# Kernel optimization log

Measured on AMD Instinct MI355X. Metric: run time of the kernel, lower is better.

## Reference

```python
import jax, jax.numpy as jnp
import numpy as np

D_MODEL = 4096
N_TYPES = 6  # fixed event_types list in the module


def setup_inputs() -> dict:
    key = jax.random.key(0)
    ks = jax.random.split(key, 7)
    E, B, d = 131072, 16384, D_MODEL
    return {
        "event_type": jax.random.randint(ks[0], (E,), 0, N_TYPES),
        "confidence": jax.random.uniform(ks[1], (E,), jnp.float32),
        "location": jax.random.uniform(ks[2], (E, 2), jnp.float32) * jnp.array([640.0, 480.0], jnp.float32),
        "batch_idx": jax.random.randint(ks[3], (E,), 0, B),
        "batch_size": B,
        "type_emb": jax.random.normal(ks[4], (N_TYPES, d // 4), jnp.float32),
        "W1": jax.random.normal(ks[5], (d // 2, d // 4 + 3), jnp.float32) / np.sqrt(d // 4 + 3).astype(np.float32),
        "b1": jnp.zeros((d // 2,), jnp.float32),
        "W2": jax.random.normal(ks[6], (d, d // 2), jnp.float32) / np.sqrt(d // 2).astype(np.float32),
        "b2": jnp.zeros((d,), jnp.float32),
    }


def reference(event_type, confidence, location, batch_idx, batch_size, type_emb, W1, b1, W2, b2):
    E = confidence.shape[0]
    B = batch_size
    # per-batch-slot max confidence (empty slots -> -inf)
    seg_max = jax.ops.segment_max(confidence, batch_idx, num_segments=B)
    is_top = confidence == seg_max[batch_idx]
    # first event attaining the max (matches torch's max-over-list semantics)
    cand = jnp.where(is_top, jnp.arange(E), E)
    top_idx = jnp.full((B,), E, dtype=cand.dtype).at[batch_idx].min(cand)
    has_event = top_idx < E
    safe_idx = jnp.where(has_event, top_idx, 0)

    emb = type_emb[event_type[safe_idx]]                 # [B, d/4]
    c = confidence[safe_idx][:, None]                    # [B, 1]
    loc = location[safe_idx] / jnp.array([640.0, 480.0], jnp.float32)  # [B, 2]
    feats = jnp.concatenate([emb, c, loc], axis=-1)      # [B, d/4 + 3]

    h = jax.nn.relu(feats @ W1.T + b1)                   # [B, d/2]
    out = h @ W2.T + b2                                  # [B, d]
    return jnp.where(has_event[:, None], out, jnp.zeros((), out.dtype))
```

## Files before the change

kernel.cpp:

```cpp
#include <hip/hip_runtime.h>
#include <hip/hip_bf16.h>

#define NT 6
#define BM 256
#define BN 256
#define BK 32
#define SLOT 16384

typedef __attribute__((ext_vector_type(4))) float f32x4;
typedef __attribute__((ext_vector_type(8))) short bf16x8;

__device__ __forceinline__ short f2bf(float f) {
    __hip_bfloat16 h = __float2bfloat16(f);
    return (short)__builtin_bit_cast(unsigned short, h);
}

__global__ void k_segmax(const float* __restrict__ conf,
                         const int* __restrict__ bidx,
                         unsigned long long* __restrict__ packed, int E) {
    int i = blockIdx.x * blockDim.x + threadIdx.x;
    if (i >= E) return;
    unsigned cb = __float_as_uint(conf[i]);
    unsigned long long p = ((unsigned long long)cb << 32) | (unsigned)(~(unsigned)i);
    atomicMax(&packed[bidx[i]], p);
}

__global__ void k_base(const float* __restrict__ emb, const float* __restrict__ W1,
                       const float* __restrict__ b1, float* __restrict__ base,
                       float* __restrict__ vecs, int d2, int d4) {
    int gw = (blockIdx.x * blockDim.x + threadIdx.x) >> 6;
    int lane = threadIdx.x & 63;
    int t = gw / d2, n = gw % d2;
    const float* e = emb + (size_t)t * d4;
    const float* w = W1 + (size_t)n * (d4 + 3);
    float s = 0.f;
    for (int k = lane; k < d4; k += 64) s += e[k] * w[k];
#pragma unroll
    for (int m = 32; m; m >>= 1) s += __shfl_xor(s, m);
    if (lane == 0) {
        base[gw] = s + b1[n];
        if (t == 0) {
            vecs[n]          = w[d4];
            vecs[d2 + n]     = w[d4 + 1];
            vecs[2 * d2 + n] = w[d4 + 2];
        }
    }
}

__global__ void k_w2cast(const float* __restrict__ W2, short* __restrict__ W2b, long n) {
    long i = ((long)blockIdx.x * blockDim.x + threadIdx.x) * 8;
    if (i >= n) return;
    bf16x8 v;
#pragma unroll
    for (int j = 0; j < 8; ++j) v[j] = f2bf(W2[i + j]);
    *(bf16x8*)(W2b + i) = v;
}

__global__ void k_h(const unsigned long long* __restrict__ packed,
                    const int* __restrict__ etype, const float* __restrict__ loc,
                    const float* __restrict__ base, const float* __restrict__ vecs,
                    float* __restrict__ mask, short* __restrict__ h, int d2) {
    int b = blockIdx.x;
    int tid = threadIdx.x;
    unsigned long long p = packed[b];
    bool has = (p != 0ULL);
    float conf = 0.f, lx = 0.f, ly = 0.f;
    int t = 0;
    if (has) {
        unsigned idx = ~(unsigned)(p & 0xFFFFFFFFu);
        conf = __uint_as_float((unsigned)(p >> 32));
        t  = etype[idx];
        lx = loc[2 * (size_t)idx]     * (1.0f / 640.0f);
        ly = loc[2 * (size_t)idx + 1] * (1.0f / 480.0f);
    }
    if (tid == 0) mask[b] = has ? 1.0f : 0.0f;
    const float* bs = base + (size_t)t * d2;
    const float* cv = vecs;
    const float* xv = vecs + d2;
    const float* yv = vecs + 2 * d2;
    int n0 = tid * 8;
    bf16x8 v;
#pragma unroll
    for (int j = 0; j < 8; ++j) {
        int n = n0 + j;
        float g = bs[n] + conf * cv[n] + lx * xv[n] + ly * yv[n];
        g = fmaxf(g, 0.f);
        v[j] = has ? f2bf(g) : (short)0;
    }
    *(bf16x8*)(h + (size_t)b * d2 + n0) = v;
}


#define GLL(src, dst) __builtin_amdgcn_global_load_lds(                      \
    (const __attribute__((address_space(1))) void*)(src),                    \
    (__attribute__((address_space(3))) void*)(dst), 16, 0, 0)

#define STAGE4(slotp) do {                                                   \
    GLL(pa0, (slotp) + dA0); GLL(pa1, (slotp) + dA1);                        \
    GLL(pb0, (slotp) + dB0); GLL(pb1, (slotp) + dB1);                        \
    pa0 += BK; pa1 += BK; pb0 += BK; pb1 += BK; } while (0)

#define SB __builtin_amdgcn_sched_barrier(0)

#define TILE(T) do {                                                         \
    const short* sr_ = lds + ((T) & 3) * SLOT;                               \
    bf16x8 bv[4], a03[4], a47[4];                                            \
    _Pragma("unroll") for (int n = 0; n < 4; ++n)                            \
        bv[n] = *(const bf16x8*)(sr_ + boff + n * 512);                      \
    _Pragma("unroll") for (int m = 0; m < 4; ++m)                            \
        a03[m] = *(const bf16x8*)(sr_ + aoff + m * 512);                     \
    _Pragma("unroll") for (int m = 0; m < 4; ++m)                            \
        a47[m] = *(const bf16x8*)(sr_ + aoff + 2048 + m * 512);              \
    if ((T) + 2 < KT) { short* sw_ = lds + (((T) + 2) & 3) * SLOT;           \
                        STAGE4(sw_); }                                       \
    __builtin_amdgcn_s_setprio(1);                                           \
    _Pragma("unroll") for (int m = 0; m < 4; ++m)                            \
    _Pragma("unroll") for (int n = 0; n < 4; ++n)                            \
        acc[m][n] = __builtin_amdgcn_mfma_f32_16x16x32_bf16(                 \
            a03[m], bv[n], acc[m][n], 0, 0, 0);                              \
    _Pragma("unroll") for (int m = 0; m < 4; ++m)                            \
    _Pragma("unroll") for (int n = 0; n < 4; ++n)                            \
        acc[4 + m][n] = __builtin_amdgcn_mfma_f32_16x16x32_bf16(             \
            a47[m], bv[n], acc[4 + m][n], 0, 0, 0);                          \
    __builtin_amdgcn_s_setprio(0);                                           \
} while (0)

__global__ __launch_bounds__(512, 2)
void k_gemm(const short* __restrict__ A, const short* __restrict__ Bm,
            const float* __restrict__ b2, const float* __restrict__ mask,
            float* __restrict__ C, int M, int N, int K, int nbn) {
    __shared__ __align__(16) short lds[4 * SLOT];

    int tid = threadIdx.x;
    int lane = tid & 63;
    int wave = tid >> 6;
    int wr = wave >> 2, wc = wave & 3;

    int bid = blockIdx.x;
    int wg = (bid & 7) * ((int)gridDim.x >> 3) + (bid >> 3);
    int bm = wg / nbn, bn = wg % nbn;
    int row0 = bm * BM, col0 = bn * BN;

    int srow = tid >> 2;
    int chunkL = (tid & 3) ^ ((srow >> 1) & 3);
    const short* pa0 = A + (size_t)(row0 + srow) * K + chunkL * 8;
    const short* pa1 = pa0 + (size_t)128 * K;
    const short* pb0 = Bm + (size_t)(col0 + srow) * K + chunkL * 8;
    const short* pb1 = pb0 + (size_t)128 * K;
    int dA0 = tid * 8, dA1 = 4096 + tid * 8;
    int dB0 = 8192 + tid * 8, dB1 = 12288 + tid * 8;

    int frow = lane & 15, fk = lane >> 4;
    int cp = fk ^ ((frow >> 1) & 3);
    int aoff = (wr * 128 + frow) * 32 + cp * 8;
    int boff = 8192 + (wc * 64 + frow) * 32 + cp * 8;

    f32x4 acc[8][4] = {};

    int KT = K / BK;

    STAGE4(lds + 0 * SLOT);
    STAGE4(lds + 1 * SLOT);
    asm volatile("s_waitcnt vmcnt(0)" ::: "memory");
    __builtin_amdgcn_s_barrier();
    SB;

#pragma unroll 1
    for (int t = 0; t < KT; t += 2) {
        TILE(t);
        TILE(t + 1);
        SB;
        if (t + 2 < KT) {
            asm volatile("s_waitcnt vmcnt(0)" ::: "memory");
            __builtin_amdgcn_s_barrier();
            SB;
        }
    }

#pragma unroll
    for (int m = 0; m < 8; ++m) {
        int rbase = row0 + wr * 128 + m * 16 + (lane >> 4) * 4;
#pragma unroll
        for (int j = 0; j < 4; ++j) {
            int r = rbase + j;
            float mk = mask[r];
#pragma unroll
            for (int n = 0; n < 4; ++n) {
                int c = col0 + wc * 64 + n * 16 + frow;
                C[(size_t)r * N + c] = (acc[m][n][j] + b2[c]) * mk;
            }
        }
    }
}

extern "C" void kernel_launch(void* const* d_in, const int* in_sizes, int n_in,
                              void* d_out, int out_size, void* d_ws, size_t ws_size,
                              hipStream_t stream) {
    const int* etype   = (const int*)d_in[0];
    const float* conf  = (const float*)d_in[1];
    const float* loc   = (const float*)d_in[2];
    const int* bidx    = (const int*)d_in[3];
    const float* emb   = (const float*)d_in[5];
    const float* W1    = (const float*)d_in[6];
    const float* b1    = (const float*)d_in[7];
    const float* W2    = (const float*)d_in[8];
    const float* b2    = (const float*)d_in[9];
    float* out = (float*)d_out;

    int E  = in_sizes[0];
    int d2 = in_sizes[7];
    int d  = in_sizes[9];
    int d4 = in_sizes[5] / NT;
    int B  = out_size / d;

    char* ws = (char*)d_ws;
    unsigned long long* packed = (unsigned long long*)ws;
    float* mask = (float*)(ws + (size_t)B * 8);
    float* base = mask + B;
    float* vecs = base + NT * d2;
    short* w2b  = (short*)(vecs + 3 * d2);
    short* h    = w2b + (size_t)d * d2;

    hipMemsetAsync(packed, 0, (size_t)B * 8, stream);
    k_segmax<<<(E + 255) / 256, 256, 0, stream>>>(conf, bidx, packed, E);
    k_base<<<(NT * d2) / 4, 256, 0, stream>>>(emb, W1, b1, base, vecs, d2, d4);
    long nw2 = (long)d * d2;
    k_w2cast<<<(int)(nw2 / 8 / 256), 256, 0, stream>>>(W2, w2b, nw2);
    k_h<<<B, 256, 0, stream>>>(packed, etype, loc, base, vecs, mask, h, d2);
    int nbm = B / BM, nbn = d / BN;
    k_gemm<<<dim3(nbm * nbn), dim3(512), 0, stream>>>(h, w2b, b2, mask, out, B, d, d2, nbn);
}
```

Measured before the change: 307.8 us.

## Double-buffer LDS fragment reads in registers to overlap with MFMA

The bf16 GEMM main loop is restructured so the LDS fragments for the next K-tile are read into a second register set while the MFMAs for the current tile run. Global-to-LDS staging is reordered around this, and a wait-plus-barrier is added after each tile instead of after every pair of tiles. The goal is to hide LDS read latency behind matrix math. In exchange it roughly doubles fragment register use and shortens how long global prefetches have to complete, which may cause spills or stalls at the vmcnt waits.

Result: slower. 320.7 us (+4.2%).

```diff
diff --git a/kernel.cpp b/kernel.cpp
--- a/kernel.cpp
+++ b/kernel.cpp
@@ -102,26 +102,26 @@
 
 #define SB __builtin_amdgcn_sched_barrier(0)
 
-#define TILE(T) do {                                                         \
+#define READF(T, BV, AL, AH) do {                                            \
     const short* sr_ = lds + ((T) & 3) * SLOT;                               \
-    bf16x8 bv[4], a03[4], a47[4];                                            \
     _Pragma("unroll") for (int n = 0; n < 4; ++n)                            \
-        bv[n] = *(const bf16x8*)(sr_ + boff + n * 512);                      \
-    _Pragma("unroll") for (int m = 0; m < 4; ++m)                            \
-        a03[m] = *(const bf16x8*)(sr_ + aoff + m * 512);                     \
-    _Pragma("unroll") for (int m = 0; m < 4; ++m)                            \
-        a47[m] = *(const bf16x8*)(sr_ + aoff + 2048 + m * 512);              \
-    if ((T) + 2 < KT) { short* sw_ = lds + (((T) + 2) & 3) * SLOT;           \
-                        STAGE4(sw_); }                                       \
+        BV[n] = *(const bf16x8*)(sr_ + boff + n * 512);                      \
+    _Pragma("unroll") for (int m = 0; m < 4; ++m)                            \
+        AL[m] = *(const bf16x8*)(sr_ + aoff + m * 512);                      \
+    _Pragma("unroll") for (int m = 0; m < 4; ++m)                            \
+        AH[m] = *(const bf16x8*)(sr_ + aoff + 2048 + m * 512);               \
+} while (0)
+
+#define MM(BV, AL, AH) do {                                                  \
     __builtin_amdgcn_s_setprio(1);                                           \
     _Pragma("unroll") for (int m = 0; m < 4; ++m)                            \
     _Pragma("unroll") for (int n = 0; n < 4; ++n)                            \
         acc[m][n] = __builtin_amdgcn_mfma_f32_16x16x32_bf16(                 \
-            a03[m], bv[n], acc[m][n], 0, 0, 0);                              \
+            AL[m], BV[n], acc[m][n], 0, 0, 0);                               \
     _Pragma("unroll") for (int m = 0; m < 4; ++m)                            \
     _Pragma("unroll") for (int n = 0; n < 4; ++n)                            \
         acc[4 + m][n] = __builtin_amdgcn_mfma_f32_16x16x32_bf16(             \
-            a47[m], bv[n], acc[4 + m][n], 0, 0, 0);                          \
+            AH[m], BV[n], acc[4 + m][n], 0, 0, 0);                           \
     __builtin_amdgcn_s_setprio(0);                                           \
 } while (0)
 
@@ -156,6 +156,7 @@
     int boff = 8192 + (wc * 64 + frow) * 32 + cp * 8;
 
     f32x4 acc[8][4] = {};
+    bf16x8 bvX[4], aXl[4], aXh[4], bvY[4], aYl[4], aYh[4];
 
     int KT = K / BK;
 
@@ -164,13 +165,29 @@
     asm volatile("s_waitcnt vmcnt(0)" ::: "memory");
     __builtin_amdgcn_s_barrier();
     SB;
+    READF(0, bvX, aXl, aXh);
 
 #pragma unroll 1
     for (int t = 0; t < KT; t += 2) {
-        TILE(t);
-        TILE(t + 1);
-        SB;
-        if (t + 2 < KT) {
+        bool more = (t + 2 < KT);
+        if (more) STAGE4(lds + ((t + 2) & 3) * SLOT);
+        READF(t + 1, bvY, aYl, aYh);
+        SB;
+        MM(bvX, aXl, aXh);
+        SB;
+        if (more) {
+            asm volatile("s_waitcnt vmcnt(0)" ::: "memory");
+            __builtin_amdgcn_s_barrier();
+            SB;
+        }
+        if (more) {
+            STAGE4(lds + ((t + 3) & 3) * SLOT);
+            READF(t + 2, bvX, aXl, aXh);
+        }
+        SB;
+        MM(bvY, aYl, aYh);
+        SB;
+        if (more) {
             asm volatile("s_waitcnt vmcnt(0)" ::: "memory");
             __builtin_amdgcn_s_barrier();
             SB;
```

## Deepen GEMM prefetch to three stages and stagger waves for LDS/MFMA overlap

Applied to the files above, without the earlier changes.

Restructures the main GEMM loop to prefetch three K-tiles ahead with a partial vmcnt wait instead of draining all loads, and syncs every tile instead of every two. Waves in the two row halves are staggered: one half reads LDS fragments then does MFMAs, while the other does MFMAs and then reads the next tile's fragments, so LDS reads and matrix ops from different waves interleave. The aim is to hide global-load latency and LDS read latency behind MFMA work. In exchange it adds a barrier per tile, keeps fragment registers live across iterations, and removes the sched_barriers, so the compiler may reorder the code differently.

Result: slower. 327.4 us (+6.4%).

```diff
diff --git a/kernel.cpp b/kernel.cpp
--- a/kernel.cpp
+++ b/kernel.cpp
@@ -100,19 +100,17 @@
     GLL(pb0, (slotp) + dB0); GLL(pb1, (slotp) + dB1);                        \
     pa0 += BK; pa1 += BK; pb0 += BK; pb1 += BK; } while (0)
 
-#define SB __builtin_amdgcn_sched_barrier(0)
-
-#define TILE(T) do {                                                         \
+#define READF(T) do {                                                        \
     const short* sr_ = lds + ((T) & 3) * SLOT;                               \
-    bf16x8 bv[4], a03[4], a47[4];                                            \
     _Pragma("unroll") for (int n = 0; n < 4; ++n)                            \
         bv[n] = *(const bf16x8*)(sr_ + boff + n * 512);                      \
     _Pragma("unroll") for (int m = 0; m < 4; ++m)                            \
         a03[m] = *(const bf16x8*)(sr_ + aoff + m * 512);                     \
     _Pragma("unroll") for (int m = 0; m < 4; ++m)                            \
         a47[m] = *(const bf16x8*)(sr_ + aoff + 2048 + m * 512);              \
-    if ((T) + 2 < KT) { short* sw_ = lds + (((T) + 2) & 3) * SLOT;           \
-                        STAGE4(sw_); }                                       \
+} while (0)
+
+#define MM do {                                                              \
     __builtin_amdgcn_s_setprio(1);                                           \
     _Pragma("unroll") for (int m = 0; m < 4; ++m)                            \
     _Pragma("unroll") for (int n = 0; n < 4; ++n)                            \
@@ -156,24 +154,32 @@
     int boff = 8192 + (wc * 64 + frow) * 32 + cp * 8;
 
     f32x4 acc[8][4] = {};
+    bf16x8 bv[4], a03[4], a47[4];
 
     int KT = K / BK;
 
     STAGE4(lds + 0 * SLOT);
     STAGE4(lds + 1 * SLOT);
-    asm volatile("s_waitcnt vmcnt(0)" ::: "memory");
+    STAGE4(lds + 2 * SLOT);
+    asm volatile("s_waitcnt vmcnt(4)" ::: "memory");
     __builtin_amdgcn_s_barrier();
-    SB;
+
+    if (wr == 1) READF(0);
 
 #pragma unroll 1
-    for (int t = 0; t < KT; t += 2) {
-        TILE(t);
-        TILE(t + 1);
-        SB;
-        if (t + 2 < KT) {
-            asm volatile("s_waitcnt vmcnt(0)" ::: "memory");
+    for (int t = 0; t < KT; ++t) {
+        if (t + 3 < KT) STAGE4(lds + ((t + 3) & 3) * SLOT);
+        if (wr == 0) {
+            READF(t);
+            MM;
+        } else {
+            MM;
+            if (t + 1 < KT) READF(t + 1);
+        }
+        if (t < KT - 1) {
+            if (t + 3 < KT) asm volatile("s_waitcnt vmcnt(4)" ::: "memory");
+            else            asm volatile("s_waitcnt vmcnt(0)" ::: "memory");
             __builtin_amdgcn_s_barrier();
-            SB;
         }
     }
 
```
